# Kernel optimization log

Measured on AMD Instinct MI355X. Metric: run time of the kernel, lower is better.

The kernel has to match this reference:

```python
import jax, jax.numpy as jnp
import numpy as np

T_MAX = 0.5
LN_EPS = 1e-5
B, N, D = 256, 16384, 512
NNZ = N * 33  # ~ (2*top_k+1) nonzeros per row of the sparse Laplacian
DF = 4 * D
DT = 32  # time-embedding hidden size


def _layernorm(x, g, b):
    mu = jnp.mean(x, axis=-1, keepdims=True)
    var = jnp.mean((x - mu) ** 2, axis=-1, keepdims=True)
    return (x - mu) * jax.lax.rsqrt(var + LN_EPS) * g + b


def setup_inputs() -> dict:
    key = jax.random.key(0)
    ks = jax.random.split(key, 16)

    def lin_w(k, fan_out, fan_in):
        return jax.random.normal(k, (fan_out, fan_in), jnp.float32) * (1.0 / np.sqrt(fan_in))

    inp = {}
    inp["x0"] = jax.random.uniform(ks[0], (B, N), jnp.float32)
    inp["t"] = jax.random.uniform(ks[1], (B,), jnp.float32)
    inp["L_vals"] = jax.random.normal(ks[2], (NNZ,), jnp.float32) * 0.1
    inp["W_in"] = lin_w(ks[3], D, N)
    inp["b_in"] = jnp.zeros((D,), jnp.float32)
    inp["W_out"] = lin_w(ks[4], N, D)
    inp["b_out"] = jnp.zeros((N,), jnp.float32)
    inp["W_qkv"] = lin_w(ks[5], 3 * D, D)
    inp["b_qkv"] = jnp.zeros((3 * D,), jnp.float32)
    inp["W_o"] = lin_w(ks[6], D, D)
    inp["b_o"] = jnp.zeros((D,), jnp.float32)
    inp["g1"] = jnp.ones((D,), jnp.float32)
    inp["be1"] = jnp.zeros((D,), jnp.float32)
    inp["g2"] = jnp.ones((D,), jnp.float32)
    inp["be2"] = jnp.zeros((D,), jnp.float32)
    inp["W_f1"] = lin_w(ks[7], DF, D)
    inp["b_f1"] = jnp.zeros((DF,), jnp.float32)
    inp["W_f2"] = lin_w(ks[8], D, DF)
    inp["b_f2"] = jnp.zeros((D,), jnp.float32)
    inp["W_t1"] = lin_w(ks[9], DT, 1)
    inp["b_t1"] = jnp.zeros((DT,), jnp.float32)
    inp["W_t2"] = lin_w(ks[10], D, DT)
    inp["b_t2"] = jnp.zeros((D,), jnp.float32)
    inp["L_rows"] = jax.random.randint(ks[11], (NNZ,), 0, N, jnp.int32)
    inp["L_cols"] = jax.random.randint(ks[12], (NNZ,), 0, N, jnp.int32)
    return inp


def reference(x0, t, L_vals, W_in, b_in, W_out, b_out, W_qkv, b_qkv, W_o, b_o,
              g1, be1, g2, be2, W_f1, b_f1, W_f2, b_f2, W_t1, b_t1, W_t2, b_t2,
              L_rows, L_cols):
    n_items = x0.shape[1]
    d_model = W_in.shape[0]
    t_cont = t * T_MAX  # per-sample diffusion time (explicit input, not RNG)

    # Batched sparse Laplacian diffusion (replaces the per-row torch.sparse.mm loop):
    # (L @ x.T)[i, b] = sum_e L_vals[e] * x0[b, L_cols[e]] aggregated to row L_rows[e]
    contrib = x0[:, L_cols] * L_vals                                  # (B, NNZ)
    Lx = jax.ops.segment_sum(contrib.T, L_rows, num_segments=n_items)  # (N, B)
    x_t = x0 - t_cont[:, None] * Lx.T                                  # (B, N)

    # Denoiser (eval mode: dropout off)
    h = x_t @ W_in.T + b_in                                            # (B, D)
    t_norm = t_cont / T_MAX
    te = jax.nn.silu(t_norm[:, None] @ W_t1.T + b_t1) @ W_t2.T + b_t2  # (B, D)
    h = h + te

    # MultiheadAttention on a length-1 sequence: softmax over one key is exactly 1,
    # so attn_out = out_proj(V) with V = h @ W_v.T + b_v.
    qkv = h @ W_qkv.T + b_qkv                                          # (B, 3D)
    v = qkv[:, 2 * d_model:]
    attn_out = v @ W_o.T + b_o

    h = _layernorm(h + attn_out, g1, be1)
    ff = jax.nn.gelu(h @ W_f1.T + b_f1, approximate=False) @ W_f2.T + b_f2
    h = _layernorm(h + ff, g2, be2)

    pred = h @ W_out.T + b_out                                         # (B, N)
    return jnp.mean((pred - x0) ** 2)
```

## Files before the change

### kernel.cpp

```cpp
#include <hip/hip_runtime.h>
#include <math.h>

#define Bb   256
#define Nn   16384
#define Dd   512
#define NNZn 540672
#define DFf  2048
#define SLOT 64

#define CVT_BLKS 4736
#define TR_BLKS  1024
#define BK_BLKS  2112

#define C1 65536
#define C2 131072
#define C3 393216
#define C4 655360
#define C5 2752512
#define C6 4849664

typedef __bf16 bf16;
typedef __bf16 bf16x4 __attribute__((ext_vector_type(4)));
typedef __bf16 bf16x8 __attribute__((ext_vector_type(8)));
typedef float  f32x4  __attribute__((ext_vector_type(4)));

__device__ __forceinline__ void gload16(const void* g, void* l) {
  __builtin_amdgcn_global_load_lds(
      (const __attribute__((address_space(1))) unsigned int*)g,
      (__attribute__((address_space(3))) unsigned int*)l, 16, 0, 0);
}

template <int NK>
__device__ __forceinline__ void bar_keep() {
  asm volatile("s_waitcnt vmcnt(%0) lgkmcnt(0)" :: "n"(NK) : "memory");
  __builtin_amdgcn_s_barrier();
}

__global__ __launch_bounds__(256) void k_prep(
    const float* __restrict__ w_v, const float* __restrict__ w_o,
    const float* __restrict__ w_f1, const float* __restrict__ w_f2,
    const float* __restrict__ w_in, const float* __restrict__ w_out,
    bf16* __restrict__ o_v, bf16* __restrict__ o_o,
    bf16* __restrict__ o_f1, bf16* __restrict__ o_f2,
    bf16* __restrict__ o_in, bf16* __restrict__ o_out,
    const float* __restrict__ x0, bf16* __restrict__ x0T,
    const int* __restrict__ rows, const int* __restrict__ cols,
    const float* __restrict__ vals,
    int* __restrict__ counts, unsigned* __restrict__ ents) {
  __shared__ float tile[64][65];
  int blk = blockIdx.x;
  if (blk < CVT_BLKS) {
    int v0i = blk * 1024 + threadIdx.x;
#pragma unroll
    for (int j = 0; j < 4; j++) {
      int v = v0i + j * 256;
      const float* s; bf16* d; int base;
      if (v < C2)      { if (v < C1) { s = w_v;  d = o_v;  base = 0;  }
                         else        { s = w_o;  d = o_o;  base = C1; } }
      else if (v < C4) { if (v < C3) { s = w_f1; d = o_f1; base = C2; }
                         else        { s = w_f2; d = o_f2; base = C3; } }
      else             { if (v < C5) { s = w_in; d = o_in; base = C4; }
                         else        { s = w_out; d = o_out; base = C5; } }
      int idx = (v - base) * 4;
      float4 x = *(const float4*)(s + idx);
      bf16x4 o;
      o[0] = (bf16)x.x; o[1] = (bf16)x.y; o[2] = (bf16)x.z; o[3] = (bf16)x.w;
      *(bf16x4*)(d + idx) = o;
    }
  } else if (blk < CVT_BLKS + TR_BLKS) {
    int bx = blk - CVT_BLKS;
    int n0 = (bx & 255) * 64, b0 = (bx >> 8) * 64;
    int tx = threadIdx.x & 63, ty = threadIdx.x >> 6;
#pragma unroll
    for (int i = 0; i < 16; i++) {
      int bl = ty * 16 + i;
      tile[bl][tx] = x0[(size_t)(b0 + bl) * Nn + n0 + tx];
    }
    __syncthreads();
#pragma unroll
    for (int i = 0; i < 16; i++) {
      int nl = ty * 16 + i;
      x0T[(size_t)(n0 + nl) * Bb + b0 + tx] = (bf16)tile[tx][nl];
    }
  } else {
    int i = (blk - CVT_BLKS - TR_BLKS) * 256 + threadIdx.x;
    int r = rows[i];
    int p = atomicAdd(&counts[r], 1);
    if (p < SLOT) {
      _Float16 hv = (_Float16)vals[i];
      unsigned short us;
      __builtin_memcpy(&us, &hv, 2);
      ents[(size_t)r * SLOT + p] = ((unsigned)cols[i] << 16) | (unsigned)us;
    }
  }
}

__global__ __launch_bounds__(256) void k_lx(const bf16x4* __restrict__ x0T4,
                                            const int* __restrict__ counts,
                                            const unsigned* __restrict__ ents,
                                            bf16x4* __restrict__ Lx4) {
  int w = threadIdx.x >> 6, lane = threadIdx.x & 63;
  int r = blockIdx.x * 4 + w;
  __shared__ unsigned esm[4][64];
  int cnt = counts[r];
  if (cnt > SLOT) cnt = SLOT;
  const unsigned* ep = ents + (size_t)r * SLOT;
  float a0 = 0.f, a1 = 0.f, a2 = 0.f, a3 = 0.f;
  float b0 = 0.f, b1 = 0.f, b2 = 0.f, b3 = 0.f;
  for (int base = 0; base < cnt; base += 64) {
    int m = cnt - base; if (m > 64) m = 64;
    if (lane < m) esm[w][lane] = ep[base + lane];
    int i = 0;
    for (; i + 1 < m; i += 2) {
      unsigned e0 = esm[w][i], e1 = esm[w][i + 1];
      bf16x4 xv0 = x0T4[(size_t)(e0 >> 16) * 64 + lane];
      bf16x4 xv1 = x0T4[(size_t)(e1 >> 16) * 64 + lane];
      unsigned short u0 = (unsigned short)(e0 & 0xffff);
      unsigned short u1 = (unsigned short)(e1 & 0xffff);
      _Float16 h0, h1;
      __builtin_memcpy(&h0, &u0, 2);
      __builtin_memcpy(&h1, &u1, 2);
      float v0 = (float)h0, v1 = (float)h1;
      a0 += v0 * (float)xv0[0]; a1 += v0 * (float)xv0[1];
      a2 += v0 * (float)xv0[2]; a3 += v0 * (float)xv0[3];
      b0 += v1 * (float)xv1[0]; b1 += v1 * (float)xv1[1];
      b2 += v1 * (float)xv1[2]; b3 += v1 * (float)xv1[3];
    }
    if (i < m) {
      unsigned e0 = esm[w][i];
      bf16x4 xv0 = x0T4[(size_t)(e0 >> 16) * 64 + lane];
      unsigned short u0 = (unsigned short)(e0 & 0xffff);
      _Float16 h0;
      __builtin_memcpy(&h0, &u0, 2);
      float v0 = (float)h0;
      a0 += v0 * (float)xv0[0]; a1 += v0 * (float)xv0[1];
      a2 += v0 * (float)xv0[2]; a3 += v0 * (float)xv0[3];
    }
  }
  bf16x4 o;
  o[0] = (bf16)(a0 + b0); o[1] = (bf16)(a1 + b1);
  o[2] = (bf16)(a2 + b2); o[3] = (bf16)(a3 + b3);
  Lx4[(size_t)r * 64 + lane] = o;
}

__global__ __launch_bounds__(256) void k_combine(const float* __restrict__ x0,
                                                 const bf16* __restrict__ Lx,
                                                 const float* __restrict__ t,
                                                 bf16* __restrict__ xt) {
  __shared__ float lxs[64][65];
  int n0 = blockIdx.x * 64, b0 = blockIdx.y * 64;
  int tx = threadIdx.x & 63, ty = threadIdx.x >> 6;
#pragma unroll
  for (int i = 0; i < 16; i++) {
    int nl = ty * 16 + i;
    lxs[nl][tx] = (float)Lx[(size_t)(n0 + nl) * Bb + b0 + tx];
  }
  __syncthreads();
#pragma unroll
  for (int i = 0; i < 16; i++) {
    int bl = ty * 16 + i;
    int b  = b0 + bl;
    float tc = t[b] * 0.5f;
    float v = x0[(size_t)b * Nn + n0 + tx] - tc * lxs[tx][bl];
    xt[(size_t)b * Nn + n0 + tx] = (bf16)v;
  }
}

template <int BM, int BN, int MODE, int ACT = 0>
__global__ __launch_bounds__(256) void gemm_tn(
    const bf16* __restrict__ A, const bf16* __restrict__ Bm,
    float* __restrict__ C, int N, int K, int kLen, int MN,
    const float* __restrict__ bias, const float* __restrict__ x0,
    float* __restrict__ lossOut) {
  constexpr int WM = BM / 2, WN = BN / 2, FM = WM / 16, FN = WN / 16;
  constexpr int PASS = (BM + BN) / 64;
  constexpr int KEEP = PASS;
  __shared__ __align__(16) bf16 As[3][BM * 32];
  __shared__ __align__(16) bf16 Bs[3][BN * 32];
  __shared__ float lred[4];
  const int tid = threadIdx.x;
  const int lane = tid & 63, w = tid >> 6;
  const int wm = w >> 1, wn = w & 1;
  const int mBase = blockIdx.x * BM, nBase = blockIdx.y * BN;
  const int k0 = blockIdx.z * kLen;
  const int nIter = kLen >> 5;

  f32x4 acc[FM][FN];
#pragma unroll
  for (int i = 0; i < FM; i++)
#pragma unroll
    for (int j = 0; j < FN; j++) acc[i][j] = {0.f, 0.f, 0.f, 0.f};

  auto stage = [&](int buf, int k) {
#pragma unroll
    for (int p = 0; p < PASS; p++) {
      int c = p * 4 + w;
      int u = c * 64 + lane;
      if (c < BM / 16) {
        int row = u >> 2, sub = u & 3;
        gload16(A + (size_t)(mBase + row) * K + k + sub * 8,
                (char*)As[buf] + c * 1024);
      } else {
        int u2 = u - BM * 4;
        int row = u2 >> 2, sub = u2 & 3;
        gload16(Bm + (size_t)(nBase + row) * K + k + sub * 8,
                (char*)Bs[buf] + (c - BM / 16) * 1024);
      }
    }
  };
  auto compute = [&](int cur) {
    bf16x8 af[FM], bfr[FN];
#pragma unroll
    for (int i = 0; i < FM; i++)
      af[i] = *(const bf16x8*)(As[cur] + (wm * WM + i * 16 + (lane & 15)) * 32 + (lane >> 4) * 8);
#pragma unroll
    for (int j = 0; j < FN; j++)
      bfr[j] = *(const bf16x8*)(Bs[cur] + (wn * WN + j * 16 + (lane & 15)) * 32 + (lane >> 4) * 8);
#pragma unroll
    for (int i = 0; i < FM; i++)
#pragma unroll
      for (int j = 0; j < FN; j++)
        acc[i][j] = __builtin_amdgcn_mfma_f32_16x16x32_bf16(af[i], bfr[j], acc[i][j], 0, 0, 0);
  };

  stage(0, k0);
  if (nIter > 1) {
    stage(1, k0 + 32);
    bar_keep<KEEP>();
  } else {
    bar_keep<0>();
  }

  int c0 = 0, c1 = 1, c2 = 2;
  for (int t = 0; t < nIter; t += 2) {
    {
      const bool more2 = (t + 2 < nIter);
      if (more2) stage(c2, k0 + (t + 2) * 32);
      compute(c0);
      if (more2) bar_keep<KEEP>(); else bar_keep<0>();
    }
    {
      const bool more2 = (t + 3 < nIter);
      if (more2) stage(c0, k0 + (t + 3) * 32);
      compute(c1);
      if (more2) bar_keep<KEEP>(); else bar_keep<0>();
    }
    int tmp = c2; c2 = c1; c1 = c0; c0 = tmp;
  }

  if constexpr (MODE == 0) {
    float* Cz = C + (size_t)blockIdx.z * MN;
#pragma unroll
    for (int i = 0; i < FM; i++)
#pragma unroll
      for (int j = 0; j < FN; j++) {
        int n  = nBase + wn * WN + j * 16 + (lane & 15);
        int mB = mBase + wm * WM + i * 16 + ((lane >> 4) << 2);
#pragma unroll
        for (int r = 0; r < 4; r++)
          Cz[(size_t)(mB + r) * N + n] = acc[i][j][r];
      }
  } else if constexpr (MODE == 1) {
    bf16* Cb = (bf16*)C;
#pragma unroll
    for (int i = 0; i < FM; i++)
#pragma unroll
      for (int j = 0; j < FN; j++) {
        int n  = nBase + wn * WN + j * 16 + (lane & 15);
        float bo = bias[n];
        int mB = mBase + wm * WM + i * 16 + ((lane >> 4) << 2);
#pragma unroll
        for (int r = 0; r < 4; r++) {
          float x = acc[i][j][r] + bo;
          if constexpr (ACT == 1)
            x = 0.5f * x * (1.f + erff(x * 0.70710678118654752f));
          Cb[(size_t)(mB + r) * N + n] = (bf16)x;
        }
      }
  } else {
    float lsum = 0.f;
#pragma unroll
    for (int i = 0; i < FM; i++)
#pragma unroll
      for (int j = 0; j < FN; j++) {
        int n  = nBase + wn * WN + j * 16 + (lane & 15);
        float bo = bias[n];
        int mB = mBase + wm * WM + i * 16 + ((lane >> 4) << 2);
#pragma unroll
        for (int r = 0; r < 4; r++) {
          float d = acc[i][j][r] + bo - x0[(size_t)(mB + r) * N + n];
          lsum += d * d;
        }
      }
    for (int off = 32; off > 0; off >>= 1) lsum += __shfl_down(lsum, off, 64);
    if (lane == 0) lred[w] = lsum;
    __syncthreads();
    if (tid == 0)
      atomicAdd(lossOut, lred[0] + lred[1] + lred[2] + lred[3]);
  }
}

__global__ __launch_bounds__(512) void k_epi_h(const float* __restrict__ P,
                                               const float* __restrict__ t,
                                               const float* __restrict__ W_t1,
                                               const float* __restrict__ b_t1,
                                               const float* __restrict__ W_t2,
                                               const float* __restrict__ b_t2,
                                               const float* __restrict__ b_in,
                                               float* __restrict__ h_f32,
                                               bf16* __restrict__ h_b) {
  int b = blockIdx.x, d = threadIdx.x;
  __shared__ float s[32];
  if (d < 32) {
    float z = t[b] * W_t1[d] + b_t1[d];
    s[d] = z / (1.f + expf(-z));
  }
  __syncthreads();
  int i = b * Dd + d;
  float v = b_in[d] + b_t2[d];
#pragma unroll
  for (int sp = 0; sp < 32; sp++) v += P[sp * (Bb * Dd) + i];
#pragma unroll
  for (int j = 0; j < 32; j++) v += s[j] * W_t2[d * 32 + j];
  h_f32[i] = v;
  h_b[i] = (bf16)v;
}

template <int NS>
__global__ __launch_bounds__(512) void k_ln(const float* __restrict__ base,
                                            const float* __restrict__ add,
                                            const float* __restrict__ bias,
                                            const float* __restrict__ g,
                                            const float* __restrict__ be,
                                            float* __restrict__ out_f32,
                                            bf16* __restrict__ out_b) {
  int b = blockIdx.x, d = threadIdx.x;
  __shared__ float red[16];
  int i = b * Dd + d;
  float x = base[i] + bias[d];
#pragma unroll
  for (int sp = 0; sp < NS; sp++) x += add[sp * (Bb * Dd) + i];
  int w = d >> 6, lane = d & 63;
  float s = x;
  for (int off = 32; off > 0; off >>= 1) s += __shfl_down(s, off, 64);
  if (lane == 0) red[w] = s;
  __syncthreads();
  if (d == 0) {
    float tot = 0.f;
    for (int q = 0; q < 8; q++) tot += red[q];
    red[8] = tot * (1.f / 512.f);
  }
  __syncthreads();
  float mu = red[8];
  float c = x - mu;
  float s2 = c * c;
  for (int off = 32; off > 0; off >>= 1) s2 += __shfl_down(s2, off, 64);
  if (lane == 0) red[w] = s2;
  __syncthreads();
  if (d == 0) {
    float tot = 0.f;
    for (int q = 0; q < 8; q++) tot += red[q];
    red[8] = tot * (1.f / 512.f);
  }
  __syncthreads();
  float var = red[8];
  float y = c * rsqrtf(var + 1e-5f) * g[d] + be[d];
  if (out_f32) out_f32[i] = y;
  out_b[i] = (bf16)y;
}

__global__ void k_final(const float* __restrict__ loss, float* __restrict__ out) {
  if (threadIdx.x == 0 && blockIdx.x == 0)
    out[0] = loss[0] * (1.f / 4194304.f);
}

extern "C" void kernel_launch(void* const* d_in, const int* in_sizes, int n_in,
                              void* d_out, int out_size, void* d_ws, size_t ws_size,
                              hipStream_t stream) {
  const float* x0    = (const float*)d_in[0];
  const float* t     = (const float*)d_in[1];
  const float* Lv    = (const float*)d_in[2];
  const float* W_in  = (const float*)d_in[3];
  const float* b_in  = (const float*)d_in[4];
  const float* W_out = (const float*)d_in[5];
  const float* b_out = (const float*)d_in[6];
  const float* W_qkv = (const float*)d_in[7];
  const float* b_qkv = (const float*)d_in[8];
  const float* W_o   = (const float*)d_in[9];
  const float* b_o   = (const float*)d_in[10];
  const float* g1    = (const float*)d_in[11];
  const float* be1   = (const float*)d_in[12];
  const float* g2    = (const float*)d_in[13];
  const float* be2   = (const float*)d_in[14];
  const float* W_f1  = (const float*)d_in[15];
  const float* b_f1  = (const float*)d_in[16];
  const float* W_f2  = (const float*)d_in[17];
  const float* b_f2  = (const float*)d_in[18];
  const float* W_t1  = (const float*)d_in[19];
  const float* b_t1  = (const float*)d_in[20];
  const float* W_t2  = (const float*)d_in[21];
  const float* b_t2  = (const float*)d_in[22];
  const int* L_rows  = (const int*)d_in[23];
  const int* L_cols  = (const int*)d_in[24];

  size_t off = 0;
  char* ws = (char*)d_ws;
  auto carve = [&](size_t bytes) -> void* {
    void* p = ws + off;
    off += (bytes + 255) & ~(size_t)255;
    return p;
  };

  bf16* W_v_b    = (bf16*)carve((size_t)Dd * Dd * 2);
  bf16* W_o_b    = (bf16*)carve((size_t)Dd * Dd * 2);
  bf16* W_f1_b   = (bf16*)carve((size_t)DFf * Dd * 2);
  bf16* W_f2_b   = (bf16*)carve((size_t)Dd * DFf * 2);
  bf16* W_in_b   = (bf16*)carve((size_t)Dd * Nn * 2);
  bf16* W_out_b  = (bf16*)carve((size_t)Nn * Dd * 2);
  bf16* x0T_b    = (bf16*)carve((size_t)Nn * Bb * 2);
  bf16* Lx_b     = (bf16*)carve((size_t)Nn * Bb * 2);
  bf16* xt_b     = (bf16*)carve((size_t)Bb * Nn * 2);
  float* p_h     = (float*)carve((size_t)32 * Bb * Dd * 4);
  float* p_at    = (float*)carve((size_t)Bb * Dd * 4);
  float* p_f2    = (float*)carve((size_t)4 * Bb * Dd * 4);
  float* h_f32   = (float*)carve((size_t)Bb * Dd * 4);
  bf16* h_b      = (bf16*)carve((size_t)Bb * Dd * 2);
  bf16* v_b      = (bf16*)carve((size_t)Bb * Dd * 2);
  float* hln_f32 = (float*)carve((size_t)Bb * Dd * 4);
  bf16* hln_b    = (bf16*)carve((size_t)Bb * Dd * 2);
  bf16* f1_b     = (bf16*)carve((size_t)Bb * DFf * 2);
  bf16* h2_b     = (bf16*)carve((size_t)Bb * Dd * 2);
  int* counts    = (int*)carve((size_t)Nn * 4);
  float* lossw   = (float*)carve(256);
  unsigned* ents = (unsigned*)carve((size_t)Nn * SLOT * 4);
  (void)in_sizes; (void)n_in; (void)out_size; (void)ws_size; (void)Lv;

  hipMemsetAsync(counts, 0, (size_t)Nn * 4 + 256, stream);

  k_prep<<<CVT_BLKS + TR_BLKS + BK_BLKS, 256, 0, stream>>>(
      W_qkv + (size_t)2 * Dd * Dd, W_o, W_f1, W_f2, W_in, W_out,
      W_v_b, W_o_b, W_f1_b, W_f2_b, W_in_b, W_out_b,
      x0, x0T_b, L_rows, L_cols, Lv, counts, ents);

  k_lx<<<Nn / 4, 256, 0, stream>>>((const bf16x4*)x0T_b, counts, ents,
                                   (bf16x4*)Lx_b);
  k_combine<<<dim3(256, 4), 256, 0, stream>>>(x0, Lx_b, t, xt_b);

  gemm_tn<64, 64, 0><<<dim3(4, 8, 32), 256, 0, stream>>>(
      xt_b, W_in_b, p_h, Dd, Nn, 512, Bb * Dd, nullptr, nullptr, nullptr);
  k_epi_h<<<Bb, 512, 0, stream>>>(p_h, t, W_t1, b_t1, W_t2, b_t2, b_in, h_f32, h_b);

  gemm_tn<32, 32, 1><<<dim3(8, 16, 1), 256, 0, stream>>>(
      h_b, W_v_b, (float*)v_b, Dd, Dd, 512, 0, b_qkv + 2 * Dd, nullptr, nullptr);

  gemm_tn<32, 32, 0><<<dim3(8, 16, 1), 256, 0, stream>>>(
      v_b, W_o_b, p_at, Dd, Dd, 512, 0, nullptr, nullptr, nullptr);
  k_ln<1><<<Bb, 512, 0, stream>>>(h_f32, p_at, b_o, g1, be1, hln_f32, hln_b);

  gemm_tn<32, 32, 1, 1><<<dim3(8, 64, 1), 256, 0, stream>>>(
      hln_b, W_f1_b, (float*)f1_b, DFf, Dd, 512, 0, b_f1, nullptr, nullptr);

  gemm_tn<32, 32, 0><<<dim3(8, 16, 4), 256, 0, stream>>>(
      f1_b, W_f2_b, p_f2, Dd, DFf, 512, Bb * Dd, nullptr, nullptr, nullptr);
  k_ln<4><<<Bb, 512, 0, stream>>>(hln_f32, p_f2, b_f2, g2, be2, nullptr, h2_b);

  gemm_tn<64, 64, 2><<<dim3(4, 256, 1), 256, 0, stream>>>(
      h2_b, W_out_b, nullptr, Nn, Dd, 512, 0, b_out, x0, lossw);
  k_final<<<1, 64, 0, stream>>>(lossw, (float*)d_out);
}
```

Baseline: 309.5 us.

## Interleave prep block types, unroll sparse gather by four, enlarge GEMM M tiles

Interleaves the atomic bucketing blocks with the conversion and transpose blocks in the prep kernel, so the contended atomic work is spread across the launch instead of running at the tail. Unrolls the sparse Laplacian gather loop to four independent accumulators, putting more loads in flight per wave. Switches the W_in and W_out GEMMs to 128x64 tiles, halving the grid in that dimension to increase operand reuse. The larger tiles may lower occupancy and parallelism, and the gemm_tn template must already support a 128 tile size.

```diff
diff --git a/kernel.cpp b/kernel.cpp
--- a/kernel.cpp
+++ b/kernel.cpp
@@ -11,6 +11,7 @@
 #define CVT_BLKS 4736
 #define TR_BLKS  1024
 #define BK_BLKS  2112
+#define PREP_BLKS (CVT_BLKS + TR_BLKS + BK_BLKS)
 
 #define C1 65536
 #define C2 131072
@@ -34,6 +35,13 @@
 __device__ __forceinline__ void bar_keep() {
   asm volatile("s_waitcnt vmcnt(%0) lgkmcnt(0)" :: "n"(NK) : "memory");
   __builtin_amdgcn_s_barrier();
+}
+
+__device__ __forceinline__ float f16_of(unsigned e) {
+  unsigned short us = (unsigned short)(e & 0xffff);
+  _Float16 h;
+  __builtin_memcpy(&h, &us, 2);
+  return (float)h;
 }
 
 __global__ __launch_bounds__(256) void k_prep(
@@ -49,41 +57,9 @@
     int* __restrict__ counts, unsigned* __restrict__ ents) {
   __shared__ float tile[64][65];
   int blk = blockIdx.x;
-  if (blk < CVT_BLKS) {
-    int v0i = blk * 1024 + threadIdx.x;
-#pragma unroll
-    for (int j = 0; j < 4; j++) {
-      int v = v0i + j * 256;
-      const float* s; bf16* d; int base;
-      if (v < C2)      { if (v < C1) { s = w_v;  d = o_v;  base = 0;  }
-                         else        { s = w_o;  d = o_o;  base = C1; } }
-      else if (v < C4) { if (v < C3) { s = w_f1; d = o_f1; base = C2; }
-                         else        { s = w_f2; d = o_f2; base = C3; } }
-      else             { if (v < C5) { s = w_in; d = o_in; base = C4; }
-                         else        { s = w_out; d = o_out; base = C5; } }
-      int idx = (v - base) * 4;
-      float4 x = *(const float4*)(s + idx);
-      bf16x4 o;
-      o[0] = (bf16)x.x; o[1] = (bf16)x.y; o[2] = (bf16)x.z; o[3] = (bf16)x.w;
-      *(bf16x4*)(d + idx) = o;
-    }
-  } else if (blk < CVT_BLKS + TR_BLKS) {
-    int bx = blk - CVT_BLKS;
-    int n0 = (bx & 255) * 64, b0 = (bx >> 8) * 64;
-    int tx = threadIdx.x & 63, ty = threadIdx.x >> 6;
-#pragma unroll
-    for (int i = 0; i < 16; i++) {
-      int bl = ty * 16 + i;
-      tile[bl][tx] = x0[(size_t)(b0 + bl) * Nn + n0 + tx];
-    }
-    __syncthreads();
-#pragma unroll
-    for (int i = 0; i < 16; i++) {
-      int nl = ty * 16 + i;
-      x0T[(size_t)(n0 + nl) * Bb + b0 + tx] = (bf16)tile[tx][nl];
-    }
-  } else {
-    int i = (blk - CVT_BLKS - TR_BLKS) * 256 + threadIdx.x;
+  int q = blk / 3;
+  if ((blk % 3) == 0 && q < BK_BLKS) {
+    int i = q * 256 + threadIdx.x;
     int r = rows[i];
     int p = atomicAdd(&counts[r], 1);
     if (p < SLOT) {
@@ -91,6 +67,43 @@
       unsigned short us;
       __builtin_memcpy(&us, &hv, 2);
       ents[(size_t)r * SLOT + p] = ((unsigned)cols[i] << 16) | (unsigned)us;
+    }
+  } else {
+    int sB = (blk + 2) / 3; if (sB > BK_BLKS) sB = BK_BLKS;
+    int o = blk - sB;
+    if (o < CVT_BLKS) {
+      int v0i = o * 1024 + threadIdx.x;
+#pragma unroll
+      for (int j = 0; j < 4; j++) {
+        int v = v0i + j * 256;
+        const float* s; bf16* d; int base;
+        if (v < C2)      { if (v < C1) { s = w_v;  d = o_v;  base = 0;  }
+                           else        { s = w_o;  d = o_o;  base = C1; } }
+        else if (v < C4) { if (v < C3) { s = w_f1; d = o_f1; base = C2; }
+                           else        { s = w_f2; d = o_f2; base = C3; } }
+        else             { if (v < C5) { s = w_in; d = o_in; base = C4; }
+                           else        { s = w_out; d = o_out; base = C5; } }
+        int idx = (v - base) * 4;
+        float4 x = *(const float4*)(s + idx);
+        bf16x4 ob;
+        ob[0] = (bf16)x.x; ob[1] = (bf16)x.y; ob[2] = (bf16)x.z; ob[3] = (bf16)x.w;
+        *(bf16x4*)(d + idx) = ob;
+      }
+    } else {
+      int bx = o - CVT_BLKS;
+      int n0 = (bx & 255) * 64, b0 = (bx >> 8) * 64;
+      int tx = threadIdx.x & 63, ty = threadIdx.x >> 6;
+#pragma unroll
+      for (int i = 0; i < 16; i++) {
+        int bl = ty * 16 + i;
+        tile[bl][tx] = x0[(size_t)(b0 + bl) * Nn + n0 + tx];
+      }
+      __syncthreads();
+#pragma unroll
+      for (int i = 0; i < 16; i++) {
+        int nl = ty * 16 + i;
+        x0T[(size_t)(n0 + nl) * Bb + b0 + tx] = (bf16)tile[tx][nl];
+      }
     }
   }
 }
@@ -107,39 +120,40 @@
   const unsigned* ep = ents + (size_t)r * SLOT;
   float a0 = 0.f, a1 = 0.f, a2 = 0.f, a3 = 0.f;
   float b0 = 0.f, b1 = 0.f, b2 = 0.f, b3 = 0.f;
+  float c0 = 0.f, c1 = 0.f, c2 = 0.f, c3 = 0.f;
+  float d0 = 0.f, d1 = 0.f, d2 = 0.f, d3 = 0.f;
   for (int base = 0; base < cnt; base += 64) {
     int m = cnt - base; if (m > 64) m = 64;
     if (lane < m) esm[w][lane] = ep[base + lane];
     int i = 0;
-    for (; i + 1 < m; i += 2) {
-      unsigned e0 = esm[w][i], e1 = esm[w][i + 1];
+    for (; i + 3 < m; i += 4) {
+      unsigned e0 = esm[w][i],     e1 = esm[w][i + 1];
+      unsigned e2 = esm[w][i + 2], e3 = esm[w][i + 3];
       bf16x4 xv0 = x0T4[(size_t)(e0 >> 16) * 64 + lane];
       bf16x4 xv1 = x0T4[(size_t)(e1 >> 16) * 64 + lane];
-      unsigned short u0 = (unsigned short)(e0 & 0xffff);
-      unsigned short u1 = (unsigned short)(e1 & 0xffff);
-      _Float16 h0, h1;
-      __builtin_memcpy(&h0, &u0, 2);
-      __builtin_memcpy(&h1, &u1, 2);
-      float v0 = (float)h0, v1 = (float)h1;
+      bf16x4 xv2 = x0T4[(size_t)(e2 >> 16) * 64 + lane];
+      bf16x4 xv3 = x0T4[(size_t)(e3 >> 16) * 64 + lane];
+      float v0 = f16_of(e0), v1 = f16_of(e1), v2 = f16_of(e2), v3 = f16_of(e3);
       a0 += v0 * (float)xv0[0]; a1 += v0 * (float)xv0[1];
       a2 += v0 * (float)xv0[2]; a3 += v0 * (float)xv0[3];
       b0 += v1 * (float)xv1[0]; b1 += v1 * (float)xv1[1];
       b2 += v1 * (float)xv1[2]; b3 += v1 * (float)xv1[3];
-    }
-    if (i < m) {
+      c0 += v2 * (float)xv2[0]; c1 += v2 * (float)xv2[1];
+      c2 += v2 * (float)xv2[2]; c3 += v2 * (float)xv2[3];
+      d0 += v3 * (float)xv3[0]; d1 += v3 * (float)xv3[1];
+      d2 += v3 * (float)xv3[2]; d3 += v3 * (float)xv3[3];
+    }
+    for (; i < m; i++) {
       unsigned e0 = esm[w][i];
       bf16x4 xv0 = x0T4[(size_t)(e0 >> 16) * 64 + lane];
-      unsigned short u0 = (unsigned short)(e0 & 0xffff);
-      _Float16 h0;
-      __builtin_memcpy(&h0, &u0, 2);
-      float v0 = (float)h0;
+      float v0 = f16_of(e0);
       a0 += v0 * (float)xv0[0]; a1 += v0 * (float)xv0[1];
       a2 += v0 * (float)xv0[2]; a3 += v0 * (float)xv0[3];
     }
   }
   bf16x4 o;
-  o[0] = (bf16)(a0 + b0); o[1] = (bf16)(a1 + b1);
-  o[2] = (bf16)(a2 + b2); o[3] = (bf16)(a3 + b3);
+  o[0] = (bf16)(a0 + b0 + c0 + d0); o[1] = (bf16)(a1 + b1 + c1 + d1);
+  o[2] = (bf16)(a2 + b2 + c2 + d2); o[3] = (bf16)(a3 + b3 + c3 + d3);
   Lx4[(size_t)r * 64 + lane] = o;
 }
 
@@ -437,7 +451,7 @@
 
   hipMemsetAsync(counts, 0, (size_t)Nn * 4 + 256, stream);
 
-  k_prep<<<CVT_BLKS + TR_BLKS + BK_BLKS, 256, 0, stream>>>(
+  k_prep<<<PREP_BLKS, 256, 0, stream>>>(
       W_qkv + (size_t)2 * Dd * Dd, W_o, W_f1, W_f2, W_in, W_out,
       W_v_b, W_o_b, W_f1_b, W_f2_b, W_in_b, W_out_b,
       x0, x0T_b, L_rows, L_cols, Lv, counts, ents);
@@ -446,7 +460,7 @@
                                    (bf16x4*)Lx_b);
   k_combine<<<dim3(256, 4), 256, 0, stream>>>(x0, Lx_b, t, xt_b);
 
-  gemm_tn<64, 64, 0><<<dim3(4, 8, 32), 256, 0, stream>>>(
+  gemm_tn<128, 64, 0><<<dim3(2, 8, 32), 256, 0, stream>>>(
       xt_b, W_in_b, p_h, Dd, Nn, 512, Bb * Dd, nullptr, nullptr, nullptr);
   k_epi_h<<<Bb, 512, 0, stream>>>(p_h, t, W_t1, b_t1, W_t2, b_t2, b_in, h_f32, h_b);
 
@@ -464,7 +478,7 @@
       f1_b, W_f2_b, p_f2, Dd, DFf, 512, Bb * Dd, nullptr, nullptr, nullptr);
   k_ln<4><<<Bb, 512, 0, stream>>>(hln_f32, p_f2, b_f2, g2, be2, nullptr, h2_b);
 
-  gemm_tn<64, 64, 2><<<dim3(4, 256, 1), 256, 0, stream>>>(
+  gemm_tn<128, 64, 2><<<dim3(2, 256, 1), 256, 0, stream>>>(
       h2_b, W_out_b, nullptr, Nn, Dd, 512, 0, b_out, x0, lossw);
   k_final<<<1, 64, 0, stream>>>(lossw, (float*)d_out);
 }
```

New measurement: 284.2 us. -8.2%, faster.
